# Kernel optimization log

Hardware: AMD Instinct MI355X
Metric: run time of the kernel (lower is better)

## Reference

```python
import jax, jax.numpy as jnp
import numpy as np

N, F_IN, HID, HEADS, CLASSES, E = 50000, 256, 64, 4, 64, 800000
NEG_SLOPE = 0.2


def _glorot(key, shape):
    fan = shape[0] + shape[-1]
    return jax.random.normal(key, shape, jnp.float32) * jnp.sqrt(2.0 / fan)


def setup_inputs() -> dict:
    key = jax.random.key(0)
    ks = jax.random.split(key, 12)
    x = jax.random.normal(ks[0], (N, F_IN), jnp.float32)
    edge_index = jax.random.randint(ks[1], (2, E), 0, N, jnp.int32)
    d = {"x": x, "edge_index": edge_index}
    dims = [(F_IN, HID), (HEADS * HID, HID), (HEADS * HID, CLASSES)]
    k = 2
    for li, (din, dout) in enumerate(dims, start=1):
        d[f"W{li}"] = _glorot(ks[k], (din, HEADS * dout)); k += 1
        d[f"a_src{li}"] = _glorot(ks[k], (HEADS, dout)); k += 1
        d[f"a_dst{li}"] = _glorot(ks[k], (HEADS, dout)); k += 1
        bdim = HEADS * dout if li < 3 else dout
        d[f"b{li}"] = jnp.zeros((bdim,), jnp.float32)
    return d


def _gat_layer(x, src, dst, W, a_src, a_dst, b, out_dim, concat):
    n = x.shape[0]
    h = (x @ W).reshape(n, HEADS, out_dim)            # [N,H,D]
    al_s = jnp.einsum("nhd,hd->nh", h, a_src)         # [N,H]
    al_d = jnp.einsum("nhd,hd->nh", h, a_dst)
    logits = jax.nn.leaky_relu(al_s[src] + al_d[dst], NEG_SLOPE)  # [E,H]
    # segment softmax over destination nodes (self-loops guarantee non-empty)
    m = jax.ops.segment_max(logits, dst, num_segments=n)
    e = jnp.exp(logits - m[dst])
    denom = jax.ops.segment_sum(e, dst, num_segments=n)
    att = e / denom[dst]                              # [E,H]
    msg = h[src] * att[:, :, None]                    # [E,H,D]
    out = jax.ops.segment_sum(msg, dst, num_segments=n)
    out = out.reshape(n, HEADS * out_dim) if concat else out.mean(axis=1)
    return out + b


def reference(x, edge_index, W1, a_src1, a_dst1, b1, W2, a_src2, a_dst2, b2,
              W3, a_src3, a_dst3, b3):
    loop = jnp.arange(N, dtype=edge_index.dtype)
    src = jnp.concatenate([edge_index[0], loop])
    dst = jnp.concatenate([edge_index[1], loop])
    h = _gat_layer(x, src, dst, W1, a_src1, a_dst1, b1, HID, True)
    h = jax.nn.elu(h)  # dropout is identity in eval mode
    h = _gat_layer(h, src, dst, W2, a_src2, a_dst2, b2, HID, True)
    h = jax.nn.elu(h)
    h = _gat_layer(h, src, dst, W3, a_src3, a_dst3, b3, CLASSES, False)
    return jax.nn.log_softmax(h, axis=-1)
```

## Files before the change

kernel.cpp:

```cpp
#include <hip/hip_runtime.h>
#include <stdint.h>

typedef __bf16 bf16x8 __attribute__((ext_vector_type(8)));
typedef float f32x4 __attribute__((ext_vector_type(4)));
typedef unsigned short u16x8 __attribute__((ext_vector_type(8)));

__device__ __forceinline__ unsigned short f2bf(float f){
  union { float f; unsigned u; } c; c.f = f;
  unsigned u = c.u;
  unsigned r = u + 0x7FFFu + ((u >> 16) & 1u);
  return (unsigned short)(r >> 16);
}

__global__ void k_hist(const int* __restrict__ ei, int E, int Nn, int* __restrict__ counts){
  int total = E + Nn;
  for (int e = blockIdx.x*blockDim.x + threadIdx.x; e < total; e += gridDim.x*blockDim.x){
    int d = (e < E) ? ei[E + e] : (e - E);
    atomicAdd(&counts[d], 1);
  }
}

__global__ __launch_bounds__(1024) void k_scan1(const int* __restrict__ counts, int* __restrict__ rowptr,
                                                int* __restrict__ bsum, int n){
  __shared__ int wsum[17];
  int tid = threadIdx.x, lane = tid & 63, wid = tid >> 6;
  int i = blockIdx.x*1024 + tid;
  int v = (i < n) ? counts[i] : 0;
  int iv = v;
  #pragma unroll
  for (int off = 1; off < 64; off <<= 1){
    int t = __shfl_up(iv, off, 64);
    if (lane >= off) iv += t;
  }
  if (lane == 63) wsum[wid] = iv;
  __syncthreads();
  if (tid == 0){
    int run = 0;
    for (int w = 0; w < 16; ++w){ int t = wsum[w]; wsum[w] = run; run += t; }
    wsum[16] = run;
  }
  __syncthreads();
  if (i < n) rowptr[i + 1] = iv + wsum[wid];
  if (tid == 0) bsum[blockIdx.x] = wsum[16];
}

__global__ __launch_bounds__(1024) void k_scan2(int* __restrict__ bsum, int nb){
  __shared__ int wsum[17];
  int tid = threadIdx.x, lane = tid & 63, wid = tid >> 6;
  int v = (tid < nb) ? bsum[tid] : 0;
  int iv = v;
  #pragma unroll
  for (int off = 1; off < 64; off <<= 1){
    int t = __shfl_up(iv, off, 64);
    if (lane >= off) iv += t;
  }
  if (lane == 63) wsum[wid] = iv;
  __syncthreads();
  if (tid == 0){
    int run = 0;
    for (int w = 0; w < 16; ++w){ int t = wsum[w]; wsum[w] = run; run += t; }
  }
  __syncthreads();
  if (tid < nb) bsum[tid] = iv + wsum[wid] - v;
}

__global__ void k_scan3(int* __restrict__ rowptr, const int* __restrict__ bsum,
                        const int* __restrict__ counts, int* __restrict__ cursor, int n){
  int i = blockIdx.x*blockDim.x + threadIdx.x;
  if (i == 0) rowptr[0] = 0;
  if (i < n){
    int v = rowptr[i + 1] + bsum[i >> 10];
    rowptr[i + 1] = v;
    cursor[i] = v - counts[i];
  }
}

__global__ void k_scatter(const int* __restrict__ ei, int E, int Nn,
                          int* __restrict__ cursor, int* __restrict__ srcs){
  int total = E + Nn;
  for (int e = blockIdx.x*blockDim.x + threadIdx.x; e < total; e += gridDim.x*blockDim.x){
    int s, d;
    if (e < E){ s = ei[e]; d = ei[E + e]; } else { s = d = e - E; }
    int pos = atomicAdd(&cursor[d], 1);
    srcs[pos] = s;
  }
}

__global__ void k_prep(const float* __restrict__ x, unsigned short* __restrict__ xbf, int nx4, int nconv,
                       const float* __restrict__ W1, const float* __restrict__ W2,
                       const float* __restrict__ W3, unsigned short* __restrict__ wt1,
                       unsigned short* __restrict__ wt2, unsigned short* __restrict__ wt3){
  int b = blockIdx.x;
  if (b < nconv){
    int i = b*256 + threadIdx.x;
    if (i < nx4){
      float4 v = reinterpret_cast<const float4*>(x)[i];
      ushort4 o;
      o.x = f2bf(v.x); o.y = f2bf(v.y); o.z = f2bf(v.z); o.w = f2bf(v.w);
      reinterpret_cast<ushort4*>(xbf)[i] = o;
    }
  } else {
    int t = (b - nconv)*256 + threadIdx.x;
    int which = t >> 16, li = t & 65535;
    int k = li >> 8, c = li & 255;
    const float* W = (which == 0) ? W1 : (which == 1) ? W2 : W3;
    unsigned short* Wt = (which == 0) ? wt1 : (which == 1) ? wt2 : wt3;
    Wt[c*256 + k] = f2bf(W[k*256 + c]);
  }
}

__global__ __launch_bounds__(256) void k_gemm5(const unsigned short* __restrict__ A,
                                               const unsigned short* __restrict__ Wt,
                                               const float* __restrict__ asrc,
                                               const float* __restrict__ adst,
                                               unsigned short* __restrict__ H,
                                               float* __restrict__ als,
                                               float* __restrict__ ald,
                                               int Nn){
  __shared__ unsigned short As[32][264];
  int tid = threadIdx.x;
  int w = tid >> 6, lane = tid & 63;
  int r = lane & 15, kg = lane >> 4;
  int row0 = blockIdx.x * 32;

  #pragma unroll
  for (int it = 0; it < 4; ++it){
    int li = it*256 + tid;
    int rr = li >> 5, c16 = li & 31;
    int gr = row0 + rr; if (gr >= Nn) gr = Nn - 1;
    uint4 v = *reinterpret_cast<const uint4*>(A + (size_t)gr*256 + c16*8);
    *reinterpret_cast<uint4*>(&As[rr][c16*8]) = v;
  }
  __syncthreads();

  f32x4 acc[2][4] = {};
  #pragma unroll
  for (int k0 = 0; k0 < 256; k0 += 32){
    bf16x8 a0 = *reinterpret_cast<const bf16x8*>(&As[r][kg*8 + k0]);
    bf16x8 a1 = *reinterpret_cast<const bf16x8*>(&As[16 + r][kg*8 + k0]);
    #pragma unroll
    for (int c = 0; c < 4; ++c){
      bf16x8 bfr = *reinterpret_cast<const bf16x8*>(Wt + (size_t)(w*64 + c*16 + r)*256 + kg*8 + k0);
      acc[0][c] = __builtin_amdgcn_mfma_f32_16x16x32_bf16(a0, bfr, acc[0][c], 0, 0, 0);
      acc[1][c] = __builtin_amdgcn_mfma_f32_16x16x32_bf16(a1, bfr, acc[1][c], 0, 0, 0);
    }
  }

  #pragma unroll
  for (int n = 0; n < 2; ++n){
    #pragma unroll
    for (int i = 0; i < 4; ++i){
      int row = row0 + n*16 + kg*4 + i;
      if (row < Nn){
        #pragma unroll
        for (int c = 0; c < 4; ++c)
          H[(size_t)row*256 + w*64 + c*16 + r] = f2bf(acc[n][c][i]);
      }
    }
  }

  float as_c[4], ad_c[4];
  #pragma unroll
  for (int c = 0; c < 4; ++c){
    as_c[c] = asrc[w*64 + c*16 + r];
    ad_c[c] = adst[w*64 + c*16 + r];
  }
  #pragma unroll
  for (int n = 0; n < 2; ++n){
    #pragma unroll
    for (int i = 0; i < 4; ++i){
      float ps = acc[n][0][i]*as_c[0] + acc[n][1][i]*as_c[1]
               + acc[n][2][i]*as_c[2] + acc[n][3][i]*as_c[3];
      float pd = acc[n][0][i]*ad_c[0] + acc[n][1][i]*ad_c[1]
               + acc[n][2][i]*ad_c[2] + acc[n][3][i]*ad_c[3];
      #pragma unroll
      for (int off = 1; off < 16; off <<= 1){
        ps += __shfl_xor(ps, off, 64);
        pd += __shfl_xor(pd, off, 64);
      }
      int row = row0 + n*16 + kg*4 + i;
      if (r == 0 && row < Nn){
        als[row*4 + w] = ps;
        ald[row*4 + w] = pd;
      }
    }
  }
}

template<int MODE>
__global__ void k_gather3(const unsigned short* __restrict__ Hm, const int* __restrict__ rowptr,
                          const int* __restrict__ srcs, const float* __restrict__ als,
                          const float* __restrict__ ald, const float* __restrict__ bias,
                          unsigned short* __restrict__ actout, float* __restrict__ finalout, int Nn){
  int gid = blockIdx.x*blockDim.x + threadIdx.x;
  int node = gid >> 6, lane = gid & 63;
  if (node >= Nn) return;
  int half = lane >> 5;
  int l32  = lane & 31;
  int fbase = l32 * 8;
  int hd = l32 >> 3;
  unsigned voff_feat = (unsigned)(l32 * 16);

  int beg = rowptr[node], deg = rowptr[node + 1] - beg;
  float4 adv = *reinterpret_cast<const float4*>(ald + (size_t)node*4);
  float aldh = (hd == 0) ? adv.x : (hd == 1) ? adv.y : (hd == 2) ? adv.z : adv.w;

  float acc[4][8];
  #pragma unroll
  for (int u = 0; u < 4; ++u)
    #pragma unroll
    for (int i = 0; i < 8; ++i) acc[u][i] = 0.f;
  float sw = 0.f;

  const char* Hb = (const char*)Hm;
  const char* Ab = (const char*)als;

  for (int cb = 0; cb < deg; cb += 64){
    int chunk = min(64, deg - cb);
    int mysrc = (cb + lane < deg) ? srcs[beg + cb + lane] : 0;
    int jmax8 = chunk & ~7;
    int j = 0;
    for (; j < jmax8; j += 8){
      #pragma unroll
      for (int u = 0; u < 4; ++u){
        int e0 = j + 2*u;
        int sA = __builtin_amdgcn_readlane(mysrc, e0);
        int sB = __builtin_amdgcn_readlane(mysrc, e0 + 1);
        int sM = half ? sB : sA;
        uint4 hw = *reinterpret_cast<const uint4*>(Hb + (unsigned)sM*512u + voff_feat);
        float av = *reinterpret_cast<const float*>(Ab + ((unsigned)sM << 4) + ((unsigned)hd << 2));
        float l = av + aldh; l = l > 0.f ? l : 0.2f*l;
        float wgt = __expf(l);
        sw += wgt;
        float h0 = __uint_as_float(hw.x << 16);
        float h1 = __uint_as_float(hw.x & 0xffff0000u);
        float h2 = __uint_as_float(hw.y << 16);
        float h3 = __uint_as_float(hw.y & 0xffff0000u);
        float h4 = __uint_as_float(hw.z << 16);
        float h5 = __uint_as_float(hw.z & 0xffff0000u);
        float h6 = __uint_as_float(hw.w << 16);
        float h7 = __uint_as_float(hw.w & 0xffff0000u);
        acc[u][0] = fmaf(wgt, h0, acc[u][0]);
        acc[u][1] = fmaf(wgt, h1, acc[u][1]);
        acc[u][2] = fmaf(wgt, h2, acc[u][2]);
        acc[u][3] = fmaf(wgt, h3, acc[u][3]);
        acc[u][4] = fmaf(wgt, h4, acc[u][4]);
        acc[u][5] = fmaf(wgt, h5, acc[u][5]);
        acc[u][6] = fmaf(wgt, h6, acc[u][6]);
        acc[u][7] = fmaf(wgt, h7, acc[u][7]);
      }
    }
    for (; j < chunk; j += 2){
      int eA = j;
      int eB = (j + 1 < chunk) ? (j + 1) : j;
      int sA = __builtin_amdgcn_readlane(mysrc, eA);
      int sB = __builtin_amdgcn_readlane(mysrc, eB);
      int sM = half ? sB : sA;
      uint4 hw = *reinterpret_cast<const uint4*>(Hb + (unsigned)sM*512u + voff_feat);
      float av = *reinterpret_cast<const float*>(Ab + ((unsigned)sM << 4) + ((unsigned)hd << 2));
      float l = av + aldh; l = l > 0.f ? l : 0.2f*l;
      float wgt = __expf(l);
      if (j + half >= chunk) wgt = 0.f;
      sw += wgt;
      float h0 = __uint_as_float(hw.x << 16);
      float h1 = __uint_as_float(hw.x & 0xffff0000u);
      float h2 = __uint_as_float(hw.y << 16);
      float h3 = __uint_as_float(hw.y & 0xffff0000u);
      float h4 = __uint_as_float(hw.z << 16);
      float h5 = __uint_as_float(hw.z & 0xffff0000u);
      float h6 = __uint_as_float(hw.w << 16);
      float h7 = __uint_as_float(hw.w & 0xffff0000u);
      acc[0][0] = fmaf(wgt, h0, acc[0][0]);
      acc[0][1] = fmaf(wgt, h1, acc[0][1]);
      acc[0][2] = fmaf(wgt, h2, acc[0][2]);
      acc[0][3] = fmaf(wgt, h3, acc[0][3]);
      acc[0][4] = fmaf(wgt, h4, acc[0][4]);
      acc[0][5] = fmaf(wgt, h5, acc[0][5]);
      acc[0][6] = fmaf(wgt, h6, acc[0][6]);
      acc[0][7] = fmaf(wgt, h7, acc[0][7]);
    }
  }

  float accf[8];
  #pragma unroll
  for (int i = 0; i < 8; ++i){
    float t = acc[0][i] + acc[1][i] + acc[2][i] + acc[3][i];
    t += __shfl_xor(t, 32, 64);
    accf[i] = t;
  }
  float s = sw + __shfl_xor(sw, 32, 64);
  float inv = 1.f / s;

  if (MODE == 0){
    if (lane < 32){
      float4 b0 = *reinterpret_cast<const float4*>(bias + fbase);
      float4 b1 = *reinterpret_cast<const float4*>(bias + fbase + 4);
      float o[8];
      o[0] = accf[0]*inv + b0.x; o[1] = accf[1]*inv + b0.y;
      o[2] = accf[2]*inv + b0.z; o[3] = accf[3]*inv + b0.w;
      o[4] = accf[4]*inv + b1.x; o[5] = accf[5]*inv + b1.y;
      o[6] = accf[6]*inv + b1.z; o[7] = accf[7]*inv + b1.w;
      u16x8 pk;
      #pragma unroll
      for (int i = 0; i < 8; ++i){
        float v = o[i];
        v = v > 0.f ? v : __expf(v) - 1.f;
        pk[i] = f2bf(v);
      }
      *reinterpret_cast<u16x8*>(actout + (size_t)node*256 + fbase) = pk;
    }
  } else {
    float v[8];
    #pragma unroll
    for (int i = 0; i < 8; ++i){
      float t = accf[i]*inv;
      t += __shfl_xor(t, 8, 64);
      t += __shfl_xor(t, 16, 64);
      v[i] = t;
    }
    int k = l32 & 7;
    float4 b0 = *reinterpret_cast<const float4*>(bias + k*8);
    float4 b1 = *reinterpret_cast<const float4*>(bias + k*8 + 4);
    v[0] = v[0]*0.25f + b0.x; v[1] = v[1]*0.25f + b0.y;
    v[2] = v[2]*0.25f + b0.z; v[3] = v[3]*0.25f + b0.w;
    v[4] = v[4]*0.25f + b1.x; v[5] = v[5]*0.25f + b1.y;
    v[6] = v[6]*0.25f + b1.z; v[7] = v[7]*0.25f + b1.w;
    float mx = v[0];
    #pragma unroll
    for (int i = 1; i < 8; ++i) mx = fmaxf(mx, v[i]);
    #pragma unroll
    for (int off = 1; off < 8; off <<= 1) mx = fmaxf(mx, __shfl_xor(mx, off, 64));
    float se = 0.f;
    #pragma unroll
    for (int i = 0; i < 8; ++i) se += __expf(v[i] - mx);
    #pragma unroll
    for (int off = 1; off < 8; off <<= 1) se += __shfl_xor(se, off, 64);
    float lse = mx + __logf(se);
    if (lane < 8){
      float4 o0, o1;
      o0.x = v[0]-lse; o0.y = v[1]-lse; o0.z = v[2]-lse; o0.w = v[3]-lse;
      o1.x = v[4]-lse; o1.y = v[5]-lse; o1.z = v[6]-lse; o1.w = v[7]-lse;
      float* dst = finalout + (size_t)node*64 + lane*8;
      *reinterpret_cast<float4*>(dst)     = o0;
      *reinterpret_cast<float4*>(dst + 4) = o1;
    }
  }
}

extern "C" void kernel_launch(void* const* d_in, const int* in_sizes, int n_in,
                              void* d_out, int out_size, void* d_ws, size_t ws_size,
                              hipStream_t stream){
  const float* x     = (const float*)d_in[0];
  const int*   ei    = (const int*)  d_in[1];
  const float* W1    = (const float*)d_in[2];
  const float* asrc1 = (const float*)d_in[3];
  const float* adst1 = (const float*)d_in[4];
  const float* b1    = (const float*)d_in[5];
  const float* W2    = (const float*)d_in[6];
  const float* asrc2 = (const float*)d_in[7];
  const float* adst2 = (const float*)d_in[8];
  const float* b2    = (const float*)d_in[9];
  const float* W3    = (const float*)d_in[10];
  const float* asrc3 = (const float*)d_in[11];
  const float* adst3 = (const float*)d_in[12];
  const float* b3    = (const float*)d_in[13];
  float* out = (float*)d_out;

  int N = in_sizes[0] / 256;
  int E = in_sizes[1] / 2;

  char* p = (char*)d_ws;
  auto carve = [&](size_t bytes){ void* r = (void*)p; p += (bytes + 511) & ~(size_t)511; return r; };
  unsigned short* xbf  = (unsigned short*)carve((size_t)N*256*2);
  unsigned short* bufH = (unsigned short*)carve((size_t)N*256*2);
  unsigned short* bufB = (unsigned short*)carve((size_t)N*256*2);
  unsigned short* wt1  = (unsigned short*)carve(256*256*2);
  unsigned short* wt2  = (unsigned short*)carve(256*256*2);
  unsigned short* wt3  = (unsigned short*)carve(256*256*2);
  float* als    = (float*)carve((size_t)N*4*4);
  float* ald    = (float*)carve((size_t)N*4*4);
  int* rowptr   = (int*)carve((size_t)(N+1)*4);
  int* counts   = (int*)carve((size_t)N*4);
  int* cursor   = (int*)carve((size_t)N*4);
  int* bsum     = (int*)carve((size_t)1024*4);
  int* srcs     = (int*)carve((size_t)(E+N)*4);

  hipMemsetAsync(counts, 0, (size_t)N*4, stream);
  k_hist<<<2048, 256, 0, stream>>>(ei, E, N, counts);
  int nb = (N + 1023) / 1024;
  k_scan1<<<nb, 1024, 0, stream>>>(counts, rowptr, bsum, N);
  k_scan2<<<1, 1024, 0, stream>>>(bsum, nb);
  k_scan3<<<(N + 255)/256, 256, 0, stream>>>(rowptr, bsum, counts, cursor, N);
  k_scatter<<<2048, 256, 0, stream>>>(ei, E, N, cursor, srcs);

  int nx4 = (N*256)/4;
  int nconv = (nx4 + 255)/256;
  k_prep<<<nconv + 768, 256, 0, stream>>>(x, xbf, nx4, nconv, W1, W2, W3, wt1, wt2, wt3);

  int gemm_grid  = (N + 31) / 32;
  int nodeblocks = (N*64 + 255)/256;

  k_gemm5<<<gemm_grid, 256, 0, stream>>>(xbf, wt1, asrc1, adst1, bufH, als, ald, N);
  k_gather3<0><<<nodeblocks, 256, 0, stream>>>(bufH, rowptr, srcs, als, ald, b1, bufB, nullptr, N);
  k_gemm5<<<gemm_grid, 256, 0, stream>>>(bufB, wt2, asrc2, adst2, bufH, als, ald, N);
  k_gather3<0><<<nodeblocks, 256, 0, stream>>>(bufH, rowptr, srcs, als, ald, b2, xbf, nullptr, N);
  k_gemm5<<<gemm_grid, 256, 0, stream>>>(xbf, wt3, asrc3, adst3, bufH, als, ald, N);
  k_gather3<1><<<nodeblocks, 256, 0, stream>>>(bufH, rowptr, srcs, als, ald, b3, nullptr, out, N);
}
```

Baseline: 432.3 us.

## Fuse fp32-to-bf16 input conversion into first GEMM and prepack weights in MFMA order

Drops the separate pass that converted x from fp32 to bf16. The first GEMM now reads fp32 x directly and converts each tile while staging it into shared memory, which avoids writing and re-reading a 25 MB bf16 copy. Weights are prepacked into the per-lane MFMA fragment order so B loads are contiguous 16-byte loads per lane, and those loads are double-buffered one k-block ahead. The first GEMM now reads twice as many A bytes per block, and the double buffering uses more registers.

After: 368.7 us. -14.7%, faster.

```diff
diff --git a/kernel.cpp b/kernel.cpp
--- a/kernel.cpp
+++ b/kernel.cpp
@@ -86,31 +86,26 @@
   }
 }
 
-__global__ void k_prep(const float* __restrict__ x, unsigned short* __restrict__ xbf, int nx4, int nconv,
-                       const float* __restrict__ W1, const float* __restrict__ W2,
-                       const float* __restrict__ W3, unsigned short* __restrict__ wt1,
-                       unsigned short* __restrict__ wt2, unsigned short* __restrict__ wt3){
-  int b = blockIdx.x;
-  if (b < nconv){
-    int i = b*256 + threadIdx.x;
-    if (i < nx4){
-      float4 v = reinterpret_cast<const float4*>(x)[i];
-      ushort4 o;
-      o.x = f2bf(v.x); o.y = f2bf(v.y); o.z = f2bf(v.z); o.w = f2bf(v.w);
-      reinterpret_cast<ushort4*>(xbf)[i] = o;
-    }
-  } else {
-    int t = (b - nconv)*256 + threadIdx.x;
-    int which = t >> 16, li = t & 65535;
-    int k = li >> 8, c = li & 255;
-    const float* W = (which == 0) ? W1 : (which == 1) ? W2 : W3;
-    unsigned short* Wt = (which == 0) ? wt1 : (which == 1) ? wt2 : wt3;
-    Wt[c*256 + k] = f2bf(W[k*256 + c]);
-  }
-}
-
-__global__ __launch_bounds__(256) void k_gemm5(const unsigned short* __restrict__ A,
-                                               const unsigned short* __restrict__ Wt,
+__global__ void k_pack(const float* __restrict__ W1, const float* __restrict__ W2,
+                       const float* __restrict__ W3, unsigned short* __restrict__ p1,
+                       unsigned short* __restrict__ p2, unsigned short* __restrict__ p3){
+  int t = blockIdx.x*blockDim.x + threadIdx.x;
+  int which = t >> 13, li = t & 8191;
+  const float* W = (which == 0) ? W1 : (which == 1) ? W2 : W3;
+  unsigned short* P = (which == 0) ? p1 : (which == 1) ? p2 : p3;
+  int l = li & 63, c = (li >> 6) & 3, kb = (li >> 8) & 7, w = li >> 11;
+  int r = l & 15, kg = l >> 4;
+  int col = w*64 + c*16 + r;
+  int k0 = kb*32 + kg*8;
+  unsigned short v[8];
+  #pragma unroll
+  for (int j = 0; j < 8; ++j) v[j] = f2bf(W[(size_t)(k0 + j)*256 + col]);
+  *reinterpret_cast<uint4*>(P + (size_t)li*8) = *reinterpret_cast<const uint4*>(v);
+}
+
+template<bool AF32>
+__global__ __launch_bounds__(256) void k_gemm6(const void* __restrict__ Av,
+                                               const unsigned short* __restrict__ Bp,
                                                const float* __restrict__ asrc,
                                                const float* __restrict__ adst,
                                                unsigned short* __restrict__ H,
@@ -123,26 +118,63 @@
   int r = lane & 15, kg = lane >> 4;
   int row0 = blockIdx.x * 32;
 
+  const unsigned short* a16 = (const unsigned short*)Av;
+  const float*          a32 = (const float*)Av;
+  const unsigned short* bpw = Bp + ((size_t)w << 14);
+
+  bf16x8 bf0[4], bf1[4];
+  #pragma unroll
+  for (int c = 0; c < 4; ++c)
+    bf0[c] = *reinterpret_cast<const bf16x8*>(bpw + ((size_t)(c*64 + lane))*8);
+
   #pragma unroll
   for (int it = 0; it < 4; ++it){
     int li = it*256 + tid;
     int rr = li >> 5, c16 = li & 31;
     int gr = row0 + rr; if (gr >= Nn) gr = Nn - 1;
-    uint4 v = *reinterpret_cast<const uint4*>(A + (size_t)gr*256 + c16*8);
-    *reinterpret_cast<uint4*>(&As[rr][c16*8]) = v;
+    if (AF32){
+      const float* ap = a32 + (size_t)gr*256 + c16*8;
+      float4 v0 = *reinterpret_cast<const float4*>(ap);
+      float4 v1 = *reinterpret_cast<const float4*>(ap + 4);
+      union { uint4 q; unsigned short s[8]; } u;
+      u.s[0]=f2bf(v0.x); u.s[1]=f2bf(v0.y); u.s[2]=f2bf(v0.z); u.s[3]=f2bf(v0.w);
+      u.s[4]=f2bf(v1.x); u.s[5]=f2bf(v1.y); u.s[6]=f2bf(v1.z); u.s[7]=f2bf(v1.w);
+      *reinterpret_cast<uint4*>(&As[rr][c16*8]) = u.q;
+    } else {
+      uint4 v = *reinterpret_cast<const uint4*>(a16 + (size_t)gr*256 + c16*8);
+      *reinterpret_cast<uint4*>(&As[rr][c16*8]) = v;
+    }
   }
   __syncthreads();
 
   f32x4 acc[2][4] = {};
   #pragma unroll
-  for (int k0 = 0; k0 < 256; k0 += 32){
-    bf16x8 a0 = *reinterpret_cast<const bf16x8*>(&As[r][kg*8 + k0]);
-    bf16x8 a1 = *reinterpret_cast<const bf16x8*>(&As[16 + r][kg*8 + k0]);
-    #pragma unroll
-    for (int c = 0; c < 4; ++c){
-      bf16x8 bfr = *reinterpret_cast<const bf16x8*>(Wt + (size_t)(w*64 + c*16 + r)*256 + kg*8 + k0);
-      acc[0][c] = __builtin_amdgcn_mfma_f32_16x16x32_bf16(a0, bfr, acc[0][c], 0, 0, 0);
-      acc[1][c] = __builtin_amdgcn_mfma_f32_16x16x32_bf16(a1, bfr, acc[1][c], 0, 0, 0);
+  for (int kb = 0; kb < 8; ++kb){
+    if (kb < 7){
+      if (kb & 1){
+        #pragma unroll
+        for (int c = 0; c < 4; ++c)
+          bf0[c] = *reinterpret_cast<const bf16x8*>(bpw + ((size_t)(((kb+1)*4 + c)*64 + lane))*8);
+      } else {
+        #pragma unroll
+        for (int c = 0; c < 4; ++c)
+          bf1[c] = *reinterpret_cast<const bf16x8*>(bpw + ((size_t)(((kb+1)*4 + c)*64 + lane))*8);
+      }
+    }
+    bf16x8 a0 = *reinterpret_cast<const bf16x8*>(&As[r][kg*8 + kb*32]);
+    bf16x8 a1 = *reinterpret_cast<const bf16x8*>(&As[16 + r][kg*8 + kb*32]);
+    if (kb & 1){
+      #pragma unroll
+      for (int c = 0; c < 4; ++c){
+        acc[0][c] = __builtin_amdgcn_mfma_f32_16x16x32_bf16(a0, bf1[c], acc[0][c], 0, 0, 0);
+        acc[1][c] = __builtin_amdgcn_mfma_f32_16x16x32_bf16(a1, bf1[c], acc[1][c], 0, 0, 0);
+      }
+    } else {
+      #pragma unroll
+      for (int c = 0; c < 4; ++c){
+        acc[0][c] = __builtin_amdgcn_mfma_f32_16x16x32_bf16(a0, bf0[c], acc[0][c], 0, 0, 0);
+        acc[1][c] = __builtin_amdgcn_mfma_f32_16x16x32_bf16(a1, bf0[c], acc[1][c], 0, 0, 0);
+      }
     }
   }
 
@@ -371,12 +403,12 @@
 
   char* p = (char*)d_ws;
   auto carve = [&](size_t bytes){ void* r = (void*)p; p += (bytes + 511) & ~(size_t)511; return r; };
-  unsigned short* xbf  = (unsigned short*)carve((size_t)N*256*2);
+  unsigned short* bufA = (unsigned short*)carve((size_t)N*256*2);
   unsigned short* bufH = (unsigned short*)carve((size_t)N*256*2);
   unsigned short* bufB = (unsigned short*)carve((size_t)N*256*2);
-  unsigned short* wt1  = (unsigned short*)carve(256*256*2);
-  unsigned short* wt2  = (unsigned short*)carve(256*256*2);
-  unsigned short* wt3  = (unsigned short*)carve(256*256*2);
+  unsigned short* bp1  = (unsigned short*)carve(256*256*2);
+  unsigned short* bp2  = (unsigned short*)carve(256*256*2);
+  unsigned short* bp3  = (unsigned short*)carve(256*256*2);
   float* als    = (float*)carve((size_t)N*4*4);
   float* ald    = (float*)carve((size_t)N*4*4);
   int* rowptr   = (int*)carve((size_t)(N+1)*4);
@@ -393,17 +425,15 @@
   k_scan3<<<(N + 255)/256, 256, 0, stream>>>(rowptr, bsum, counts, cursor, N);
   k_scatter<<<2048, 256, 0, stream>>>(ei, E, N, cursor, srcs);
 
-  int nx4 = (N*256)/4;
-  int nconv = (nx4 + 255)/256;
-  k_prep<<<nconv + 768, 256, 0, stream>>>(x, xbf, nx4, nconv, W1, W2, W3, wt1, wt2, wt3);
+  k_pack<<<96, 256, 0, stream>>>(W1, W2, W3, bp1, bp2, bp3);
 
   int gemm_grid  = (N + 31) / 32;
   int nodeblocks = (N*64 + 255)/256;
 
-  k_gemm5<<<gemm_grid, 256, 0, stream>>>(xbf, wt1, asrc1, adst1, bufH, als, ald, N);
+  k_gemm6<true><<<gemm_grid, 256, 0, stream>>>(x, bp1, asrc1, adst1, bufH, als, ald, N);
   k_gather3<0><<<nodeblocks, 256, 0, stream>>>(bufH, rowptr, srcs, als, ald, b1, bufB, nullptr, N);
-  k_gemm5<<<gemm_grid, 256, 0, stream>>>(bufB, wt2, asrc2, adst2, bufH, als, ald, N);
-  k_gather3<0><<<nodeblocks, 256, 0, stream>>>(bufH, rowptr, srcs, als, ald, b2, xbf, nullptr, N);
-  k_gemm5<<<gemm_grid, 256, 0, stream>>>(xbf, wt3, asrc3, adst3, bufH, als, ald, N);
+  k_gemm6<false><<<gemm_grid, 256, 0, stream>>>(bufB, bp2, asrc2, adst2, bufH, als, ald, N);
+  k_gather3<0><<<nodeblocks, 256, 0, stream>>>(bufH, rowptr, srcs, als, ald, b2, bufA, nullptr, N);
+  k_gemm6<false><<<gemm_grid, 256, 0, stream>>>(bufA, bp3, asrc3, adst3, bufH, als, ald, N);
   k_gather3<1><<<nodeblocks, 256, 0, stream>>>(bufH, rowptr, srcs, als, ald, b3, nullptr, out, N);
 }
```
